# Kernel optimization log

Hardware: AMD Instinct MI355X
Metric: run time of the kernel (lower is better)

The kernel has to match this reference:

```python
import jax, jax.numpy as jnp
import numpy as np

ON_OFF = "off"  # init kwarg: 'off' includes the next-frame temporal candidate

def setup_inputs() -> dict:
    key = jax.random.key(0)
    k1, k2 = jax.random.split(key)
    xs = jax.random.normal(k1, (4, 32, 128, 32), dtype=jnp.float32)  # [B,T,N,D]
    A = jax.random.randint(k2, (1, 128, 128), 0, 2, dtype=jnp.int32)  # [1,N,N] adjacency
    return {"xs": xs, "A": A}

def reference(xs, A):
    B, T, N, D = xs.shape
    # A_f = A + I ; neighbors are nonzero entries (self-loop included via eye)
    A_f = A[0].astype(xs.dtype) + jnp.eye(N, dtype=xs.dtype)
    spatial_mask = A_f != 0  # [N,N] : spatial_mask[n, j] -> j is neighbor of n

    # Candidate set per (frame t, node n): prev-frame self, next-frame self (on_off=='off'),
    # and all spatial neighbors at frame t. Padded to fixed size K = N + 2 with masks.
    spat = jnp.broadcast_to(xs[:, :, None, :, :], (B, T, N, N, D))   # [B,T,N,N,D]
    prev = jnp.concatenate([xs[:, :1], xs[:, :-1]], axis=1)          # [B,T,N,D] (t=0 masked)
    nxt = jnp.concatenate([xs[:, 1:], xs[:, -1:]], axis=1)           # [B,T,N,D] (t=T-1 masked)
    cand = jnp.concatenate([prev[:, :, :, None, :], nxt[:, :, :, None, :], spat], axis=3)  # [B,T,N,N+2,D]

    t = jnp.arange(T)
    prev_m = jnp.broadcast_to((t > 0)[:, None, None], (T, N, 1))
    if ON_OFF == "off":
        next_m = jnp.broadcast_to((t < T - 1)[:, None, None], (T, N, 1))
    else:
        next_m = jnp.zeros((T, N, 1), dtype=bool)
    sp_m = jnp.broadcast_to(spatial_mask[None], (T, N, N))
    mask = jnp.concatenate([prev_m, next_m, sp_m], axis=2)  # [T,N,N+2]

    # Masked median = torch.median semantics (lower median): sort with +inf padding,
    # pick index (k-1)//2 where k = number of valid candidates.
    vals = jnp.where(mask[None, :, :, :, None], cand, jnp.inf)
    vals = jnp.sort(vals, axis=3)
    k = mask.sum(axis=2)              # [T,N]
    med_idx = (k - 1) // 2            # lower median index
    idx = jnp.broadcast_to(med_idx[None, :, :, None, None], (B, T, N, 1, D))
    ys = jnp.take_along_axis(vals, idx, axis=3)[:, :, :, 0, :]  # [B,T,N,D]
    return ys
```

## Files before the change

### kernel.cpp

```cpp
#include <hip/hip_runtime.h>
#include <stdint.h>
#include <math.h>

#define BB 4
#define TT 32
#define NN 128
#define DD 32
#define NPB 16
#define TPB (NPB * DD)
#define NBLK (BB * TT * (NN / NPB))
#define CAP 16

#define SID_PREV 0xFFFEu
#define SID_NEXT 0xFFFFu

__device__ __forceinline__ int bin8(float x) {
    int i = (int)fmaf(x, 5.0f, 4.0f);
    i = i < 0 ? 0 : i;
    return i > 7 ? 7 : i;
}

__global__ __launch_bounds__(64) void build_adj_kernel(const int* __restrict__ A,
                                                       int* __restrict__ deg,
                                                       uint8_t* __restrict__ nbr) {
    const int n = blockIdx.x;
    const int lane = threadIdx.x;
    const int* arow = A + n * NN;
    uint8_t* row = nbr + n * NN;
    const int j0 = lane, j1 = lane + 64;
    const bool b0 = (arow[j0] != 0) || (j0 == n);
    const bool b1 = (arow[j1] != 0) || (j1 == n);
    const unsigned long long m0 = __ballot(b0);
    const unsigned long long m1 = __ballot(b1);
    const unsigned long long lmask = (1ULL << lane) - 1ULL;
    const int c0 = __popcll(m0);
    if (b0) row[__popcll(m0 & lmask)] = (uint8_t)j0;
    if (b1) row[c0 + __popcll(m1 & lmask)] = (uint8_t)j1;
    if (lane == 0) deg[n] = c0 + __popcll(m1);
}

__global__ __launch_bounds__(TPB) void median_kernel(const float* __restrict__ xs,
                                                     const int* __restrict__ deg,
                                                     const uint8_t* __restrict__ nbr,
                                                     float* __restrict__ out) {
    __shared__ float sval[NN * DD];
    __shared__ uint32_t snbr_w[NPB * NN / 4];
    __shared__ int sdeg[NPB];
    __shared__ uint16_t slist[(CAP + 1) * TPB];

    const int tid = threadIdx.x;
    const int bid = blockIdx.x;
    const int g = ((bid & 7) << 7) | (bid >> 3);
    const int ng = g & (NN / NPB - 1);
    const int t  = (g >> 3) & (TT - 1);
    const int b  = g >> 8;
    const int n0 = ng * NPB;

    const int d = tid & (DD - 1);
    const int nl = tid >> 5;
    const int n = n0 + nl;
    const int pv = (t > 0) ? 1 : 0;
    const int nv = (t < TT - 1) ? 1 : 0;
    const int ne = pv + nv;

    float exv0 = 0.0f, exv1 = 0.0f;
    if (pv) exv0 = xs[(((size_t)(b * TT + t - 1) * NN) + n) * DD + d];
    if (nv) {
        float v = xs[(((size_t)(b * TT + t + 1) * NN) + n) * DD + d];
        if (pv) exv1 = v; else exv0 = v;
    }

    const float4* src4 = (const float4*)(xs + ((size_t)(b * TT + t) * NN) * DD);
    #pragma unroll
    for (int s = 0; s < 2; ++s) {
        int i4 = tid + (s << 9);
        ((float4*)sval)[i4] = src4[i4];
    }
    snbr_w[tid] = ((const uint32_t*)(nbr + (size_t)n0 * NN))[tid];
    if (tid < NPB) sdeg[tid] = deg[n0 + tid];
    __syncthreads();

    const int dg = sdeg[nl];
    const int k = dg + ne;
    const uint32_t r = (uint32_t)((k - 1) >> 1);
    const uint8_t* nb = (const uint8_t*)snbr_w + nl * NN;
    const float INFV = __uint_as_float(0x7F800000u);

    unsigned long long pcnt = 0ull;
    {
        int j = 0;
        for (; j + 4 <= dg; j += 4) {
            uint32_t nw = *(const uint32_t*)(nb + j);
            #pragma unroll
            for (int q = 0; q < 4; ++q) {
                float x = sval[((nw >> (q * 8)) & 0xFFu) * DD + d];
                pcnt += 1ull << (bin8(x) * 8);
            }
        }
        for (; j < dg; ++j) {
            float x = sval[nb[j] * DD + d];
            pcnt += 1ull << (bin8(x) * 8);
        }
        if (ne >= 1) pcnt += 1ull << (bin8(exv0) * 8);
        if (ne == 2) pcnt += 1ull << (bin8(exv1) * 8);
    }

    uint32_t cum = 0, lowcnt = 0, mexp = 0;
    int selbin = -1;
    #pragma unroll
    for (int bb = 0; bb < 8; ++bb) {
        uint32_t bc = (uint32_t)(pcnt >> (bb * 8)) & 0xFFu;
        uint32_t nc = cum + bc;
        if (selbin < 0 && r < nc) { selbin = bb; lowcnt = cum; mexp = bc; }
        cum = nc;
    }
    const bool fb = (mexp > CAP);
    const uint32_t rp = r - lowcnt;
    const int storebin = fb ? -1 : selbin;

    int mc = 0;
    {
        int j = 0;
        for (; j + 4 <= dg; j += 4) {
            uint32_t nw = *(const uint32_t*)(nb + j);
            #pragma unroll
            for (int q = 0; q < 4; ++q) {
                uint32_t id = (nw >> (q * 8)) & 0xFFu;
                float x = sval[id * DD + d];
                int slot = mc > CAP ? CAP : mc;
                slist[slot * TPB + tid] = (uint16_t)id;
                mc += (bin8(x) == storebin);
            }
        }
        for (; j < dg; ++j) {
            uint32_t id = nb[j];
            float x = sval[id * DD + d];
            int slot = mc > CAP ? CAP : mc;
            slist[slot * TPB + tid] = (uint16_t)id;
            mc += (bin8(x) == storebin);
        }
        if (ne >= 1) {
            int slot = mc > CAP ? CAP : mc;
            slist[slot * TPB + tid] = (uint16_t)SID_PREV;
            mc += (bin8(exv0) == storebin);
        }
        if (ne == 2) {
            int slot = mc > CAP ? CAP : mc;
            slist[slot * TPB + tid] = (uint16_t)SID_NEXT;
            mc += (bin8(exv1) == storebin);
        }
    }

    auto bandval = [&](int e) -> float {
        uint32_t id = slist[e * TPB + tid];
        float v = sval[(id & 127u) * DD + d];
        v = (id == SID_PREV) ? exv0 : v;
        v = (id == SID_NEXT) ? exv1 : v;
        return v;
    };

    float ki[CAP];
    uint32_t cn[CAP];
    #pragma unroll
    for (int u = 0; u < CAP; ++u) {
        float v = bandval(u);
        ki[u] = (u < mc) ? v : INFV;
        cn[u] = 0;
    }
    int mm = mc;
    #pragma unroll
    for (int off = 32; off; off >>= 1) {
        int o = __shfl_xor(mm, off);
        mm = mm > o ? mm : o;
    }
    for (int j = 0; j < mm; ++j) {
        float x = bandval(j);
        x = (j < mc) ? x : INFV;
        #pragma unroll
        for (int u = 0; u < CAP; ++u) cn[u] += (x < ki[u]);
    }
    float result = 0.0f;
    bool found = fb;
    #pragma unroll
    for (int u = 0; u < CAP; ++u) {
        if (!found && u < mc && cn[u] == rp) { result = ki[u]; found = true; }
    }

    if (__ballot(!found)) {
        uint32_t eq[CAP];
        #pragma unroll
        for (int u = 0; u < CAP; ++u) eq[u] = 0;
        for (int j = 0; j < mm; ++j) {
            float x = bandval(j);
            x = (j < mc) ? x : INFV;
            #pragma unroll
            for (int u = 0; u < CAP; ++u) eq[u] += (x == ki[u]);
        }
        #pragma unroll
        for (int u = 0; u < CAP; ++u) {
            if (!found && u < mc && cn[u] <= rp && rp < cn[u] + eq[u]) {
                result = ki[u]; found = true;
            }
        }
    }

    if (__ballot(fb)) {
        bool done = !fb;
        for (int i0 = 0; __ballot(!done && i0 < k); i0 += 8) {
            float k8[8]; uint32_t c8[8];
            #pragma unroll
            for (int u = 0; u < 8; ++u) {
                int i = i0 + u;
                float sv = sval[nb[i & 127] * DD + d];
                float ev = ((i - dg) == 0) ? exv0 : exv1;
                float v = (i < dg) ? sv : ev;
                k8[u] = (i < k) ? v : INFV;
                c8[u] = 0;
            }
            for (int j = 0; j < dg; ++j) {
                float xv = sval[nb[j] * DD + d];
                #pragma unroll
                for (int u = 0; u < 8; ++u) c8[u] += (xv < k8[u]);
            }
            if (ne >= 1) {
                #pragma unroll
                for (int u = 0; u < 8; ++u) c8[u] += (exv0 < k8[u]);
            }
            if (ne == 2) {
                #pragma unroll
                for (int u = 0; u < 8; ++u) c8[u] += (exv1 < k8[u]);
            }
            #pragma unroll
            for (int u = 0; u < 8; ++u) {
                if (!done && (i0 + u) < k && c8[u] == r) { result = k8[u]; done = true; }
            }
        }
        if (__ballot(!done)) {
            for (int i0 = 0; __ballot(!done && i0 < k); i0 += 4) {
                float k4[4]; uint32_t lt4[4], le4[4];
                #pragma unroll
                for (int u = 0; u < 4; ++u) {
                    int i = i0 + u;
                    float sv = sval[nb[i & 127] * DD + d];
                    float ev = ((i - dg) == 0) ? exv0 : exv1;
                    float v = (i < dg) ? sv : ev;
                    k4[u] = (i < k) ? v : INFV;
                    lt4[u] = 0; le4[u] = 0;
                }
                for (int j = 0; j < dg; ++j) {
                    float xv = sval[nb[j] * DD + d];
                    #pragma unroll
                    for (int u = 0; u < 4; ++u) { lt4[u] += (xv < k4[u]); le4[u] += (xv <= k4[u]); }
                }
                if (ne >= 1) {
                    #pragma unroll
                    for (int u = 0; u < 4; ++u) { lt4[u] += (exv0 < k4[u]); le4[u] += (exv0 <= k4[u]); }
                }
                if (ne == 2) {
                    #pragma unroll
                    for (int u = 0; u < 4; ++u) { lt4[u] += (exv1 < k4[u]); le4[u] += (exv1 <= k4[u]); }
                }
                #pragma unroll
                for (int u = 0; u < 4; ++u) {
                    if (!done && (i0 + u) < k && lt4[u] <= r && r < le4[u]) {
                        result = k4[u]; done = true;
                    }
                }
            }
        }
    }

    out[(((size_t)(b * TT + t) * NN) + n) * DD + d] = result;
}

extern "C" void kernel_launch(void* const* d_in, const int* in_sizes, int n_in,
                              void* d_out, int out_size, void* d_ws, size_t ws_size,
                              hipStream_t stream) {
    const float* xs = (const float*)d_in[0];
    const int* A = (const int*)d_in[1];
    float* out = (float*)d_out;

    int* deg = (int*)d_ws;
    uint8_t* nbr = (uint8_t*)d_ws + 512;

    build_adj_kernel<<<NN, 64, 0, stream>>>(A, deg, nbr);
    median_kernel<<<NBLK, TPB, 0, stream>>>(xs, deg, nbr, out);
}
```

Before: 128.0 us.

## Precompute per-value bins in shared memory and shrink candidate index lists

After: 122.3 us. 1.05x faster.

```diff
diff --git a/kernel.cpp b/kernel.cpp
--- a/kernel.cpp
+++ b/kernel.cpp
@@ -10,9 +10,10 @@
 #define TPB (NPB * DD)
 #define NBLK (BB * TT * (NN / NPB))
 #define CAP 16
-
-#define SID_PREV 0xFFFEu
-#define SID_NEXT 0xFFFFu
+#define SSTR (TPB + 4)
+
+#define SID_PREV 0xFEu
+#define SID_NEXT 0xFFu
 
 __device__ __forceinline__ int bin8(float x) {
     int i = (int)fmaf(x, 5.0f, 4.0f);
@@ -44,9 +45,10 @@
                                                      const uint8_t* __restrict__ nbr,
                                                      float* __restrict__ out) {
     __shared__ float sval[NN * DD];
+    __shared__ uint8_t sbin[NN * DD];
     __shared__ uint32_t snbr_w[NPB * NN / 4];
     __shared__ int sdeg[NPB];
-    __shared__ uint16_t slist[(CAP + 1) * TPB];
+    __shared__ uint8_t slist[(CAP + 1) * SSTR];
 
     const int tid = threadIdx.x;
     const int bid = blockIdx.x;
@@ -74,7 +76,11 @@
     #pragma unroll
     for (int s = 0; s < 2; ++s) {
         int i4 = tid + (s << 9);
-        ((float4*)sval)[i4] = src4[i4];
+        float4 f = src4[i4];
+        ((float4*)sval)[i4] = f;
+        uint32_t pk = (uint32_t)bin8(f.x) | ((uint32_t)bin8(f.y) << 8)
+                    | ((uint32_t)bin8(f.z) << 16) | ((uint32_t)bin8(f.w) << 24);
+        ((uint32_t*)sbin)[i4] = pk;
     }
     snbr_w[tid] = ((const uint32_t*)(nbr + (size_t)n0 * NN))[tid];
     if (tid < NPB) sdeg[tid] = deg[n0 + tid];
@@ -86,23 +92,28 @@
     const uint8_t* nb = (const uint8_t*)snbr_w + nl * NN;
     const float INFV = __uint_as_float(0x7F800000u);
 
+    auto gbin = [&](uint32_t id) -> int { return (int)sbin[id * DD + d]; };
+    const int be0 = bin8(exv0);
+    const int be1 = bin8(exv1);
+
     unsigned long long pcnt = 0ull;
     {
         int j = 0;
-        for (; j + 4 <= dg; j += 4) {
-            uint32_t nw = *(const uint32_t*)(nb + j);
+        for (; j + 8 <= dg; j += 8) {
+            uint32_t nw0 = *(const uint32_t*)(nb + j);
+            uint32_t nw1 = *(const uint32_t*)(nb + j + 4);
+            int bsv[8];
             #pragma unroll
             for (int q = 0; q < 4; ++q) {
-                float x = sval[((nw >> (q * 8)) & 0xFFu) * DD + d];
-                pcnt += 1ull << (bin8(x) * 8);
-            }
-        }
-        for (; j < dg; ++j) {
-            float x = sval[nb[j] * DD + d];
-            pcnt += 1ull << (bin8(x) * 8);
-        }
-        if (ne >= 1) pcnt += 1ull << (bin8(exv0) * 8);
-        if (ne == 2) pcnt += 1ull << (bin8(exv1) * 8);
+                bsv[q]     = gbin((nw0 >> (q * 8)) & 0xFFu);
+                bsv[q + 4] = gbin((nw1 >> (q * 8)) & 0xFFu);
+            }
+            #pragma unroll
+            for (int q = 0; q < 8; ++q) pcnt += 1ull << (bsv[q] * 8);
+        }
+        for (; j < dg; ++j) pcnt += 1ull << (gbin(nb[j]) * 8);
+        if (ne >= 1) pcnt += 1ull << (be0 * 8);
+        if (ne == 2) pcnt += 1ull << (be1 * 8);
     }
 
     uint32_t cum = 0, lowcnt = 0, mexp = 0;
@@ -121,38 +132,45 @@
     int mc = 0;
     {
         int j = 0;
-        for (; j + 4 <= dg; j += 4) {
-            uint32_t nw = *(const uint32_t*)(nb + j);
+        for (; j + 8 <= dg; j += 8) {
+            uint32_t nw0 = *(const uint32_t*)(nb + j);
+            uint32_t nw1 = *(const uint32_t*)(nb + j + 4);
+            uint32_t ids[8]; int bsv[8];
             #pragma unroll
             for (int q = 0; q < 4; ++q) {
-                uint32_t id = (nw >> (q * 8)) & 0xFFu;
-                float x = sval[id * DD + d];
+                ids[q]     = (nw0 >> (q * 8)) & 0xFFu;
+                ids[q + 4] = (nw1 >> (q * 8)) & 0xFFu;
+            }
+            #pragma unroll
+            for (int q = 0; q < 8; ++q) bsv[q] = gbin(ids[q]);
+            #pragma unroll
+            for (int q = 0; q < 8; ++q) {
                 int slot = mc > CAP ? CAP : mc;
-                slist[slot * TPB + tid] = (uint16_t)id;
-                mc += (bin8(x) == storebin);
+                slist[slot * SSTR + tid] = (uint8_t)ids[q];
+                mc += (bsv[q] == storebin);
             }
         }
         for (; j < dg; ++j) {
             uint32_t id = nb[j];
-            float x = sval[id * DD + d];
+            int bv = gbin(id);
             int slot = mc > CAP ? CAP : mc;
-            slist[slot * TPB + tid] = (uint16_t)id;
-            mc += (bin8(x) == storebin);
+            slist[slot * SSTR + tid] = (uint8_t)id;
+            mc += (bv == storebin);
         }
         if (ne >= 1) {
             int slot = mc > CAP ? CAP : mc;
-            slist[slot * TPB + tid] = (uint16_t)SID_PREV;
-            mc += (bin8(exv0) == storebin);
+            slist[slot * SSTR + tid] = (uint8_t)SID_PREV;
+            mc += (be0 == storebin);
         }
         if (ne == 2) {
             int slot = mc > CAP ? CAP : mc;
-            slist[slot * TPB + tid] = (uint16_t)SID_NEXT;
-            mc += (bin8(exv1) == storebin);
+            slist[slot * SSTR + tid] = (uint8_t)SID_NEXT;
+            mc += (be1 == storebin);
         }
     }
 
     auto bandval = [&](int e) -> float {
-        uint32_t id = slist[e * TPB + tid];
+        uint32_t id = slist[e * SSTR + tid];
         float v = sval[(id & 127u) * DD + d];
         v = (id == SID_PREV) ? exv0 : v;
         v = (id == SID_NEXT) ? exv1 : v;
@@ -173,11 +191,22 @@
         int o = __shfl_xor(mm, off);
         mm = mm > o ? mm : o;
     }
-    for (int j = 0; j < mm; ++j) {
-        float x = bandval(j);
-        x = (j < mc) ? x : INFV;
-        #pragma unroll
-        for (int u = 0; u < CAP; ++u) cn[u] += (x < ki[u]);
+    {
+        int j = 0;
+        for (; j + 2 <= mm; j += 2) {
+            float x0 = bandval(j);
+            float x1 = bandval(j + 1);
+            x0 = (j < mc) ? x0 : INFV;
+            x1 = (j + 1 < mc) ? x1 : INFV;
+            #pragma unroll
+            for (int u = 0; u < CAP; ++u) cn[u] += (x0 < ki[u]) + (x1 < ki[u]);
+        }
+        if (j < mm) {
+            float x = bandval(j);
+            x = (j < mc) ? x : INFV;
+            #pragma unroll
+            for (int u = 0; u < CAP; ++u) cn[u] += (x < ki[u]);
+        }
     }
     float result = 0.0f;
     bool found = fb;
```

## Replace neighbor-list scans with per-bin bitmask histograms and popcount selection

Applied to the files above, without the earlier changes.

After: 288.5 us. 125% more time.

```diff
diff --git a/kernel.cpp b/kernel.cpp
--- a/kernel.cpp
+++ b/kernel.cpp
@@ -10,9 +10,7 @@
 #define TPB (NPB * DD)
 #define NBLK (BB * TT * (NN / NPB))
 #define CAP 16
-
-#define SID_PREV 0xFFFEu
-#define SID_NEXT 0xFFFFu
+#define NK (CAP + 2)
 
 __device__ __forceinline__ int bin8(float x) {
     int i = (int)fmaf(x, 5.0f, 4.0f);
@@ -21,32 +19,22 @@
 }
 
 __global__ __launch_bounds__(64) void build_adj_kernel(const int* __restrict__ A,
-                                                       int* __restrict__ deg,
-                                                       uint8_t* __restrict__ nbr) {
+                                                       unsigned long long* __restrict__ mask) {
     const int n = blockIdx.x;
     const int lane = threadIdx.x;
     const int* arow = A + n * NN;
-    uint8_t* row = nbr + n * NN;
-    const int j0 = lane, j1 = lane + 64;
-    const bool b0 = (arow[j0] != 0) || (j0 == n);
-    const bool b1 = (arow[j1] != 0) || (j1 == n);
+    const bool b0 = (arow[lane] != 0) || (lane == n);
+    const bool b1 = (arow[lane + 64] != 0) || (lane + 64 == n);
     const unsigned long long m0 = __ballot(b0);
     const unsigned long long m1 = __ballot(b1);
-    const unsigned long long lmask = (1ULL << lane) - 1ULL;
-    const int c0 = __popcll(m0);
-    if (b0) row[__popcll(m0 & lmask)] = (uint8_t)j0;
-    if (b1) row[c0 + __popcll(m1 & lmask)] = (uint8_t)j1;
-    if (lane == 0) deg[n] = c0 + __popcll(m1);
+    if (lane == 0) { mask[n * 2] = m0; mask[n * 2 + 1] = m1; }
 }
 
 __global__ __launch_bounds__(TPB) void median_kernel(const float* __restrict__ xs,
-                                                     const int* __restrict__ deg,
-                                                     const uint8_t* __restrict__ nbr,
+                                                     const unsigned long long* __restrict__ mask,
                                                      float* __restrict__ out) {
-    __shared__ float sval[NN * DD];
-    __shared__ uint32_t snbr_w[NPB * NN / 4];
-    __shared__ int sdeg[NPB];
-    __shared__ uint16_t slist[(CAP + 1) * TPB];
+    __shared__ __align__(16) float sval[NN * DD];
+    __shared__ __align__(16) unsigned int sbit[8 * DD * 4];
 
     const int tid = threadIdx.x;
     const int bid = blockIdx.x;
@@ -70,135 +58,114 @@
         if (pv) exv1 = v; else exv0 = v;
     }
 
+    ((uint2*)sbit)[tid] = make_uint2(0u, 0u);
+
     const float4* src4 = (const float4*)(xs + ((size_t)(b * TT + t) * NN) * DD);
-    #pragma unroll
-    for (int s = 0; s < 2; ++s) {
-        int i4 = tid + (s << 9);
-        ((float4*)sval)[i4] = src4[i4];
-    }
-    snbr_w[tid] = ((const uint32_t*)(nbr + (size_t)n0 * NN))[tid];
-    if (tid < NPB) sdeg[tid] = deg[n0 + tid];
+    const float4 f0 = src4[tid];
+    const float4 f1 = src4[tid + 512];
+    ((float4*)sval)[tid] = f0;
+    ((float4*)sval)[tid + 512] = f1;
+
     __syncthreads();
 
-    const int dg = sdeg[nl];
+    {
+        const int e0 = tid * 4;
+        const int en = e0 >> 5;
+        const int ed = e0 & 31;
+        const unsigned int bm = 1u << (en & 31);
+        const int wo = en >> 5;
+        atomicOr(&sbit[bin8(f0.x) * 128 + (ed + 0) * 4 + wo], bm);
+        atomicOr(&sbit[bin8(f0.y) * 128 + (ed + 1) * 4 + wo], bm);
+        atomicOr(&sbit[bin8(f0.z) * 128 + (ed + 2) * 4 + wo], bm);
+        atomicOr(&sbit[bin8(f0.w) * 128 + (ed + 3) * 4 + wo], bm);
+        const int en1 = en + 64;
+        const unsigned int bm1 = 1u << (en1 & 31);
+        const int wo1 = en1 >> 5;
+        atomicOr(&sbit[bin8(f1.x) * 128 + (ed + 0) * 4 + wo1], bm1);
+        atomicOr(&sbit[bin8(f1.y) * 128 + (ed + 1) * 4 + wo1], bm1);
+        atomicOr(&sbit[bin8(f1.z) * 128 + (ed + 2) * 4 + wo1], bm1);
+        atomicOr(&sbit[bin8(f1.w) * 128 + (ed + 3) * 4 + wo1], bm1);
+    }
+    __syncthreads();
+
+    const uint4 am4 = *((const uint4*)(mask + (size_t)n * 2));
+    const unsigned int a0 = am4.x, a1 = am4.y, a2 = am4.z, a3 = am4.w;
+    const unsigned long long am0 = (((unsigned long long)a1) << 32) | a0;
+    const unsigned long long am1 = (((unsigned long long)a3) << 32) | a2;
+    const int dg = __popcll(am0) + __popcll(am1);
     const int k = dg + ne;
     const uint32_t r = (uint32_t)((k - 1) >> 1);
-    const uint8_t* nb = (const uint8_t*)snbr_w + nl * NN;
+    const int be0 = bin8(exv0);
+    const int be1 = bin8(exv1);
     const float INFV = __uint_as_float(0x7F800000u);
 
-    unsigned long long pcnt = 0ull;
-    {
-        int j = 0;
-        for (; j + 4 <= dg; j += 4) {
-            uint32_t nw = *(const uint32_t*)(nb + j);
-            #pragma unroll
-            for (int q = 0; q < 4; ++q) {
-                float x = sval[((nw >> (q * 8)) & 0xFFu) * DD + d];
-                pcnt += 1ull << (bin8(x) * 8);
-            }
-        }
-        for (; j < dg; ++j) {
-            float x = sval[nb[j] * DD + d];
-            pcnt += 1ull << (bin8(x) * 8);
-        }
-        if (ne >= 1) pcnt += 1ull << (bin8(exv0) * 8);
-        if (ne == 2) pcnt += 1ull << (bin8(exv1) * 8);
+    int hist[8];
+    const uint4* sbit4 = (const uint4*)sbit;
+    #pragma unroll
+    for (int bb = 0; bb < 8; ++bb) {
+        uint4 w = sbit4[bb * 32 + d];
+        hist[bb] = __popc(w.x & a0) + __popc(w.y & a1) + __popc(w.z & a2) + __popc(w.w & a3);
     }
 
     uint32_t cum = 0, lowcnt = 0, mexp = 0;
     int selbin = -1;
     #pragma unroll
     for (int bb = 0; bb < 8; ++bb) {
-        uint32_t bc = (uint32_t)(pcnt >> (bb * 8)) & 0xFFu;
+        uint32_t bc = (uint32_t)hist[bb] + ((ne >= 1 && be0 == bb) ? 1u : 0u)
+                                         + ((ne == 2 && be1 == bb) ? 1u : 0u);
         uint32_t nc = cum + bc;
         if (selbin < 0 && r < nc) { selbin = bb; lowcnt = cum; mexp = bc; }
         cum = nc;
     }
     const bool fb = (mexp > CAP);
     const uint32_t rp = r - lowcnt;
-    const int storebin = fb ? -1 : selbin;
-
-    int mc = 0;
-    {
-        int j = 0;
-        for (; j + 4 <= dg; j += 4) {
-            uint32_t nw = *(const uint32_t*)(nb + j);
-            #pragma unroll
-            for (int q = 0; q < 4; ++q) {
-                uint32_t id = (nw >> (q * 8)) & 0xFFu;
-                float x = sval[id * DD + d];
-                int slot = mc > CAP ? CAP : mc;
-                slist[slot * TPB + tid] = (uint16_t)id;
-                mc += (bin8(x) == storebin);
-            }
-        }
-        for (; j < dg; ++j) {
-            uint32_t id = nb[j];
-            float x = sval[id * DD + d];
-            int slot = mc > CAP ? CAP : mc;
-            slist[slot * TPB + tid] = (uint16_t)id;
-            mc += (bin8(x) == storebin);
-        }
-        if (ne >= 1) {
-            int slot = mc > CAP ? CAP : mc;
-            slist[slot * TPB + tid] = (uint16_t)SID_PREV;
-            mc += (bin8(exv0) == storebin);
-        }
-        if (ne == 2) {
-            int slot = mc > CAP ? CAP : mc;
-            slist[slot * TPB + tid] = (uint16_t)SID_NEXT;
-            mc += (bin8(exv1) == storebin);
-        }
-    }
-
-    auto bandval = [&](int e) -> float {
-        uint32_t id = slist[e * TPB + tid];
-        float v = sval[(id & 127u) * DD + d];
-        v = (id == SID_PREV) ? exv0 : v;
-        v = (id == SID_NEXT) ? exv1 : v;
-        return v;
-    };
-
-    float ki[CAP];
-    uint32_t cn[CAP];
+
+    const int sb = fb ? 0 : selbin;
+    uint4 ws = sbit4[sb * 32 + d];
+    unsigned long long bm0 = (((unsigned long long)(ws.y & a1)) << 32) | (ws.x & a0);
+    unsigned long long bm1 = (((unsigned long long)(ws.w & a3)) << 32) | (ws.z & a2);
+    const int mc_sp = fb ? 0 : (__popcll(bm0) + __popcll(bm1));
+
+    float ki[NK];
     #pragma unroll
     for (int u = 0; u < CAP; ++u) {
-        float v = bandval(u);
-        ki[u] = (u < mc) ? v : INFV;
-        cn[u] = 0;
-    }
-    int mm = mc;
-    #pragma unroll
-    for (int off = 32; off; off >>= 1) {
-        int o = __shfl_xor(mm, off);
-        mm = mm > o ? mm : o;
-    }
-    for (int j = 0; j < mm; ++j) {
-        float x = bandval(j);
-        x = (j < mc) ? x : INFV;
-        #pragma unroll
-        for (int u = 0; u < CAP; ++u) cn[u] += (x < ki[u]);
-    }
+        const bool lo = (bm0 != 0ull);
+        const unsigned long long mm_ = lo ? bm0 : bm1;
+        const int ff = __ffsll((unsigned long long)mm_) - 1;
+        const int id = ((lo ? ff : 64 + ff) & 127);
+        const float v = sval[id * DD + d];
+        ki[u] = (u < mc_sp) ? v : INFV;
+        const unsigned long long cl = mm_ & (mm_ - 1ull);
+        bm0 = lo ? cl : bm0;
+        bm1 = lo ? bm1 : cl;
+    }
+    const bool t0 = (ne >= 1) && (be0 == selbin) && !fb;
+    const bool t1 = (ne == 2) && (be1 == selbin) && !fb;
+    ki[CAP]     = t0 ? exv0 : INFV;
+    ki[CAP + 1] = t1 ? exv1 : INFV;
+
     float result = 0.0f;
     bool found = fb;
     #pragma unroll
-    for (int u = 0; u < CAP; ++u) {
-        if (!found && u < mc && cn[u] == rp) { result = ki[u]; found = true; }
+    for (int u = 0; u < NK; ++u) {
+        uint32_t cnu = 0;
+        #pragma unroll
+        for (int v = 0; v < NK; ++v) cnu += (ki[v] < ki[u]) ? 1u : 0u;
+        const bool valid = (u < CAP) ? (u < mc_sp) : ((u == CAP) ? t0 : t1);
+        if (!found && valid && cnu == rp) { result = ki[u]; found = true; }
     }
 
     if (__ballot(!found)) {
-        uint32_t eq[CAP];
         #pragma unroll
-        for (int u = 0; u < CAP; ++u) eq[u] = 0;
-        for (int j = 0; j < mm; ++j) {
-            float x = bandval(j);
-            x = (j < mc) ? x : INFV;
+        for (int u = 0; u < NK; ++u) {
+            uint32_t cnu = 0, equ = 0;
             #pragma unroll
-            for (int u = 0; u < CAP; ++u) eq[u] += (x == ki[u]);
-        }
-        #pragma unroll
-        for (int u = 0; u < CAP; ++u) {
-            if (!found && u < mc && cn[u] <= rp && rp < cn[u] + eq[u]) {
+            for (int v = 0; v < NK; ++v) {
+                cnu += (ki[v] < ki[u]) ? 1u : 0u;
+                equ += (ki[v] == ki[u]) ? 1u : 0u;
+            }
+            const bool valid = (u < CAP) ? (u < mc_sp) : ((u == CAP) ? t0 : t1);
+            if (!found && valid && cnu <= rp && rp < cnu + equ) {
                 result = ki[u]; found = true;
             }
         }
@@ -206,63 +173,82 @@
 
     if (__ballot(fb)) {
         bool done = !fb;
-        for (int i0 = 0; __ballot(!done && i0 < k); i0 += 8) {
+        for (int i0 = 0; __ballot(!done && i0 < NN + 2); i0 += 8) {
             float k8[8]; uint32_t c8[8];
             #pragma unroll
             for (int u = 0; u < 8; ++u) {
-                int i = i0 + u;
-                float sv = sval[nb[i & 127] * DD + d];
-                float ev = ((i - dg) == 0) ? exv0 : exv1;
-                float v = (i < dg) ? sv : ev;
-                k8[u] = (i < k) ? v : INFV;
+                const int i = i0 + u;
+                const unsigned long long src = (i < 64) ? am0 : am1;
+                const bool memsp = ((src >> (i & 63)) & 1ull) != 0ull;
+                const bool mem = (i < 128) ? memsp
+                               : ((i == 128) ? (ne >= 1) : ((i == 129) ? (ne == 2) : false));
+                const float v = (i < 128) ? sval[(i & 127) * DD + d]
+                                          : ((i == 128) ? exv0 : exv1);
+                k8[u] = mem ? v : INFV;
                 c8[u] = 0;
             }
-            for (int j = 0; j < dg; ++j) {
-                float xv = sval[nb[j] * DD + d];
-                #pragma unroll
-                for (int u = 0; u < 8; ++u) c8[u] += (xv < k8[u]);
+            for (int j = 0; j < NN; ++j) {
+                const unsigned long long srcj = (j < 64) ? am0 : am1;
+                const bool mj = ((srcj >> (j & 63)) & 1ull) != 0ull;
+                const float x = mj ? sval[j * DD + d] : INFV;
+                #pragma unroll
+                for (int u = 0; u < 8; ++u) c8[u] += (x < k8[u]) ? 1u : 0u;
             }
             if (ne >= 1) {
                 #pragma unroll
-                for (int u = 0; u < 8; ++u) c8[u] += (exv0 < k8[u]);
+                for (int u = 0; u < 8; ++u) c8[u] += (exv0 < k8[u]) ? 1u : 0u;
             }
             if (ne == 2) {
                 #pragma unroll
-                for (int u = 0; u < 8; ++u) c8[u] += (exv1 < k8[u]);
+                for (int u = 0; u < 8; ++u) c8[u] += (exv1 < k8[u]) ? 1u : 0u;
             }
             #pragma unroll
             for (int u = 0; u < 8; ++u) {
-                if (!done && (i0 + u) < k && c8[u] == r) { result = k8[u]; done = true; }
+                if (!done && k8[u] < INFV && c8[u] == r) { result = k8[u]; done = true; }
             }
         }
         if (__ballot(!done)) {
-            for (int i0 = 0; __ballot(!done && i0 < k); i0 += 4) {
+            for (int i0 = 0; __ballot(!done && i0 < NN + 2); i0 += 4) {
                 float k4[4]; uint32_t lt4[4], le4[4];
                 #pragma unroll
                 for (int u = 0; u < 4; ++u) {
-                    int i = i0 + u;
-                    float sv = sval[nb[i & 127] * DD + d];
-                    float ev = ((i - dg) == 0) ? exv0 : exv1;
-                    float v = (i < dg) ? sv : ev;
-                    k4[u] = (i < k) ? v : INFV;
+                    const int i = i0 + u;
+                    const unsigned long long src = (i < 64) ? am0 : am1;
+                    const bool memsp = ((src >> (i & 63)) & 1ull) != 0ull;
+                    const bool mem = (i < 128) ? memsp
+                                   : ((i == 128) ? (ne >= 1) : ((i == 129) ? (ne == 2) : false));
+                    const float v = (i < 128) ? sval[(i & 127) * DD + d]
+                                              : ((i == 128) ? exv0 : exv1);
+                    k4[u] = mem ? v : INFV;
                     lt4[u] = 0; le4[u] = 0;
                 }
-                for (int j = 0; j < dg; ++j) {
-                    float xv = sval[nb[j] * DD + d];
+                for (int j = 0; j < NN; ++j) {
+                    const unsigned long long srcj = (j < 64) ? am0 : am1;
+                    const bool mj = ((srcj >> (j & 63)) & 1ull) != 0ull;
+                    const float x = mj ? sval[j * DD + d] : INFV;
                     #pragma unroll
-                    for (int u = 0; u < 4; ++u) { lt4[u] += (xv < k4[u]); le4[u] += (xv <= k4[u]); }
+                    for (int u = 0; u < 4; ++u) {
+                        lt4[u] += (x < k4[u]) ? 1u : 0u;
+                        le4[u] += (x <= k4[u]) ? 1u : 0u;
+                    }
                 }
                 if (ne >= 1) {
                     #pragma unroll
-                    for (int u = 0; u < 4; ++u) { lt4[u] += (exv0 < k4[u]); le4[u] += (exv0 <= k4[u]); }
+                    for (int u = 0; u < 4; ++u) {
+                        lt4[u] += (exv0 < k4[u]) ? 1u : 0u;
+                        le4[u] += (exv0 <= k4[u]) ? 1u : 0u;
+                    }
                 }
                 if (ne == 2) {
                     #pragma unroll
-                    for (int u = 0; u < 4; ++u) { lt4[u] += (exv1 < k4[u]); le4[u] += (exv1 <= k4[u]); }
+                    for (int u = 0; u < 4; ++u) {
+                        lt4[u] += (exv1 < k4[u]) ? 1u : 0u;
+                        le4[u] += (exv1 <= k4[u]) ? 1u : 0u;
+                    }
                 }
                 #pragma unroll
                 for (int u = 0; u < 4; ++u) {
-                    if (!done && (i0 + u) < k && lt4[u] <= r && r < le4[u]) {
+                    if (!done && k4[u] < INFV && lt4[u] <= r && r < le4[u]) {
                         result = k4[u]; done = true;
                     }
                 }
@@ -280,9 +266,8 @@
     const int* A = (const int*)d_in[1];
     float* out = (float*)d_out;
 
-    int* deg = (int*)d_ws;
-    uint8_t* nbr = (uint8_t*)d_ws + 512;
-
-    build_adj_kernel<<<NN, 64, 0, stream>>>(A, deg, nbr);
-    median_kernel<<<NBLK, TPB, 0, stream>>>(xs, deg, nbr, out);
-}
+    unsigned long long* mask = (unsigned long long*)d_ws;
+
+    build_adj_kernel<<<NN, 64, 0, stream>>>(A, mask);
+    median_kernel<<<NBLK, TPB, 0, stream>>>(xs, mask, out);
+}
```
